# Optimization experiments

Hardware: AMD Instinct MI355X
Metric: run time of the kernel (lower is better)

Reference implementation:

```python
import jax, jax.numpy as jnp
import numpy as np

LAMBDA_CONT = 0.01
SIGMA = 1.0


def _pairwise_dist(x):
    # Euclidean cdist(x, x): [N, N]
    sq = jnp.sum(x * x, axis=-1)  # [N]
    d2 = sq[:, None] + sq[None, :] - 2.0 * (x @ x.T)
    d2 = jnp.maximum(d2, 0.0)
    # safe sqrt (grad 0 at 0, matching torch.cdist subgradient)
    return jnp.where(d2 > 0, jnp.sqrt(jnp.where(d2 > 0, d2, 1.0)), 0.0)


def setup_inputs() -> dict:
    key = jax.random.key(0)
    k1, k2 = jax.random.split(key)
    points = jax.random.normal(k1, (8192, 2), dtype=jnp.float32)
    outputs = jax.random.uniform(k2, (8192, 8), dtype=jnp.float32)
    return {"points": points, "outputs": outputs}


def reference(points, outputs):
    n = points.shape[0]
    dist = _pairwise_dist(points)                     # [N, N]
    weights = jnp.exp(-(dist * dist) / (2.0 * SIGMA ** 2))
    weights = weights * (1.0 - jnp.eye(n, dtype=points.dtype))
    diff = _pairwise_dist(outputs)                    # [N, N]
    loss = jnp.sum(weights * diff) / (n * (n - 1))
    return LAMBDA_CONT * loss
```

## Files before the change

kernel.cpp:

```cpp
#include <hip/hip_runtime.h>


typedef float v2f __attribute__((ext_vector_type(2)));
typedef float v4f __attribute__((ext_vector_type(4)));
typedef _Float16 h4 __attribute__((ext_vector_type(4)));
typedef float f32x4 __attribute__((ext_vector_type(4)));

constexpr int N_PTS  = 8192;
constexpr int T16    = N_PTS / 16;
constexpr int TDIM   = N_PTS / 64;
constexpr int NTILES = TDIM * (TDIM + 1) / 2;
constexpr int WPB    = 4;
constexpr int NBLOCKS = NTILES / WPB;

constexpr float KE = -0.72134752044448169f;
constexpr float M2 =  1.4426950408889634f;

__device__ __forceinline__ int tri_before(int r) {
    return r * TDIM - (r * (r - 1)) / 2;
}

__global__ __launch_bounds__(256) void cont_prep(
    const float* __restrict__ points, const float* __restrict__ outputs,
    h4* __restrict__ AO, h4* __restrict__ AP,
    h4* __restrict__ BO, h4* __restrict__ BP)
{
    const int idx = blockIdx.x * 256 + threadIdx.x;
    const int l  = idx & 63;
    const int t  = idx >> 6;
    const int q  = l >> 4, cl = l & 15;
    const int row = t * 16 + cl;

    const v4f* o = reinterpret_cast<const v4f*>(outputs + 8 * row);
    const v4f x = o[0], y = o[1];
    const v4f s = x * x + y * y;
    const float on = (s.x + s.y) + (s.z + s.w);
    const v2f p = reinterpret_cast<const v2f*>(points)[row];
    const float pn = p.x * p.x + p.y * p.y;

    const _Float16 h0 = (_Float16)0.f, h1 = (_Float16)1.f;
    h4 ao, ap, bo, bp;
    if (q == 0)      ao = h4{(_Float16)x.x, (_Float16)x.y, (_Float16)x.z, (_Float16)x.w};
    else if (q == 1) ao = h4{(_Float16)y.x, (_Float16)y.y, (_Float16)y.z, (_Float16)y.w};
    else if (q == 2) ao = h4{(_Float16)on, h1, h0, h0};
    else             ao = h4{h0, h0, h0, h0};
    if (q == 0) ap = h4{(_Float16)p.x, (_Float16)p.y, (_Float16)(KE * pn), h1};
    else        ap = h4{h0, h0, h0, h0};
    if (q == 0)      bo = h4{(_Float16)(-2.f * x.x), (_Float16)(-2.f * x.y),
                             (_Float16)(-2.f * x.z), (_Float16)(-2.f * x.w)};
    else if (q == 1) bo = h4{(_Float16)(-2.f * y.x), (_Float16)(-2.f * y.y),
                             (_Float16)(-2.f * y.z), (_Float16)(-2.f * y.w)};
    else if (q == 2) bo = h4{h1, (_Float16)on, h0, h0};
    else             bo = h4{h0, h0, h0, h0};
    if (q == 0) bp = h4{(_Float16)(M2 * p.x), (_Float16)(M2 * p.y), h1,
                        (_Float16)(KE * pn)};
    else        bp = h4{h0, h0, h0, h0};

    AO[idx] = ao; AP[idx] = ap; BO[idx] = bo; BP[idx] = bp;
}

__global__ __launch_bounds__(256, 4) void cont_pairs(
    const h4* __restrict__ AO, const h4* __restrict__ AP,
    const h4* __restrict__ BO, const h4* __restrict__ BP,
    double* __restrict__ partials)
{
    const int tid  = threadIdx.x;
    const int wid  = tid >> 6;
    const int lane = tid & 63;
    const int g    = blockIdx.x * WPB + wid;

    int ti = (int)((2 * TDIM + 1 -
                    sqrtf((float)((2 * TDIM + 1) * (2 * TDIM + 1) - 8 * g))) * 0.5f);
    ti = ti < 0 ? 0 : (ti > TDIM - 1 ? TDIM - 1 : ti);
    while (tri_before(ti + 1) <= g) ++ti;
    while (tri_before(ti) > g) --ti;
    const int tj = ti + (g - tri_before(ti));
    const bool diag = (ti == tj);

    const int q = lane >> 4, cl = lane & 15;

    h4 aO[4], aP[4], bO[4], bP[4];
    #pragma unroll
    for (int it = 0; it < 4; ++it) {
        const int ta = (ti * 4 + it) * 64 + lane;
        aO[it] = AO[ta]; aP[it] = AP[ta];
        const int tb = (tj * 4 + it) * 64 + lane;
        bO[it] = BO[tb]; bP[it] = BP[tb];
    }

    float accE[4] = {0.f, 0.f, 0.f, 0.f};

    #pragma unroll
    for (int jt = 0; jt < 4; ++jt) {
        const int jcol = jt * 16 + cl;
        #pragma unroll
        for (int it = 0; it < 4; ++it) {
            const f32x4 z = {0.f, 0.f, 0.f, 0.f};
            f32x4 dO = __builtin_amdgcn_mfma_f32_16x16x16f16(aO[it], bO[jt], z, 0, 0, 0);
            f32x4 dP = __builtin_amdgcn_mfma_f32_16x16x16f16(aP[it], bP[jt], z, 0, 0, 0);
            #pragma unroll
            for (int e = 0; e < 4; ++e) {
                float diff = __builtin_amdgcn_sqrtf(fmaxf(dO[e], 0.f));
                if (diag) {
                    const int irow = it * 16 + q * 4 + e;
                    diff = (jcol > irow) ? diff : 0.f;
                }
                accE[e] = fmaf(__builtin_amdgcn_exp2f(dP[e]), diff, accE[e]);
            }
        }
    }

    float accS = (accE[0] + accE[1]) + (accE[2] + accE[3]);
    #pragma unroll
    for (int off = 32; off > 0; off >>= 1)
        accS += __shfl_down(accS, off, 64);

    __shared__ float wpart[WPB];
    if (lane == 0) wpart[wid] = accS;
    __syncthreads();
    if (tid == 0) {
        double d = 0.0;
        #pragma unroll
        for (int w = 0; w < WPB; ++w) d += (double)wpart[w];
        partials[blockIdx.x] = d;
    }
}

__global__ __launch_bounds__(1024) void cont_final(
    const double* __restrict__ partials, int nparts,
    float* __restrict__ out, double scale)
{
    const int tid = threadIdx.x;
    double sum = 0.0;
    for (int i = tid; i < nparts; i += 1024) sum += partials[i];
    #pragma unroll
    for (int off = 32; off > 0; off >>= 1)
        sum += __shfl_down(sum, off, 64);

    __shared__ double ws[1024 / 64];
    if ((tid & 63) == 0) ws[tid >> 6] = sum;
    __syncthreads();
    if (tid == 0) {
        double t = 0.0;
        #pragma unroll
        for (int w = 0; w < 1024 / 64; ++w) t += ws[w];
        out[0] = (float)(t * scale);
    }
}

extern "C" void kernel_launch(void* const* d_in, const int* in_sizes, int n_in,
                              void* d_out, int out_size, void* d_ws, size_t ws_size,
                              hipStream_t stream) {
    const float* points  = (const float*)d_in[0];
    const float* outputs = (const float*)d_in[1];
    float* out = (float*)d_out;

    const int n = in_sizes[0] / 2;
    constexpr size_t TBL = (size_t)T16 * 64 * sizeof(h4);
    h4* AO = (h4*)d_ws;
    h4* AP = (h4*)((char*)d_ws + TBL);
    h4* BO = (h4*)((char*)d_ws + 2 * TBL);
    h4* BP = (h4*)((char*)d_ws + 3 * TBL);
    double* partials = (double*)((char*)d_ws + 4 * TBL);

    cont_prep<<<dim3(T16 * 64 / 256), dim3(256), 0, stream>>>(
        points, outputs, AO, AP, BO, BP);
    cont_pairs<<<dim3(NBLOCKS), dim3(256), 0, stream>>>(AO, AP, BO, BP, partials);

    const double scale = 0.01 * 2.0 / ((double)n * (double)(n - 1));
    cont_final<<<1, 1024, 0, stream>>>(partials, NBLOCKS, out, scale);
}
```

Before: 23.19 us.

## Use 64x128 wave tiles over upper triangle and fold final reduction into atomics

Each wave now covers a 64-row by 128-column tile of the upper triangle, with a new index mapping that pairs row tiles, instead of a 64x64 tile. This halves the number of waves and amortizes the A-fragment loads and per-wave setup over twice the MFMA work. The separate final reduction kernel is removed: each block scales its partial and atomically adds it to the float output, which is zeroed by a memset. This trades a kernel launch for float atomics, which can change summation order and precision.

Result: slower. 31.82 us (+37.2%).

```diff
diff --git a/kernel.cpp b/kernel.cpp
--- a/kernel.cpp
+++ b/kernel.cpp
@@ -8,17 +8,14 @@
 
 constexpr int N_PTS  = 8192;
 constexpr int T16    = N_PTS / 16;
-constexpr int TDIM   = N_PTS / 64;
-constexpr int NTILES = TDIM * (TDIM + 1) / 2;
+constexpr int NWAVES = 4160;
 constexpr int WPB    = 4;
-constexpr int NBLOCKS = NTILES / WPB;
+constexpr int NBLOCKS = NWAVES / WPB;
 
 constexpr float KE = -0.72134752044448169f;
 constexpr float M2 =  1.4426950408889634f;
 
-__device__ __forceinline__ int tri_before(int r) {
-    return r * TDIM - (r * (r - 1)) / 2;
-}
+__device__ __forceinline__ int rp_before(int h) { return h * (129 - h); }
 
 __global__ __launch_bounds__(256) void cont_prep(
     const float* __restrict__ points, const float* __restrict__ outputs,
@@ -62,37 +59,43 @@
 __global__ __launch_bounds__(256, 4) void cont_pairs(
     const h4* __restrict__ AO, const h4* __restrict__ AP,
     const h4* __restrict__ BO, const h4* __restrict__ BP,
-    double* __restrict__ partials)
+    float* __restrict__ out, double scale)
 {
     const int tid  = threadIdx.x;
     const int wid  = tid >> 6;
     const int lane = tid & 63;
     const int g    = blockIdx.x * WPB + wid;
 
-    int ti = (int)((2 * TDIM + 1 -
-                    sqrtf((float)((2 * TDIM + 1) * (2 * TDIM + 1) - 8 * g))) * 0.5f);
-    ti = ti < 0 ? 0 : (ti > TDIM - 1 ? TDIM - 1 : ti);
-    while (tri_before(ti + 1) <= g) ++ti;
-    while (tri_before(ti) > g) --ti;
-    const int tj = ti + (g - tri_before(ti));
-    const bool diag = (ti == tj);
+    int h = (int)((129.f - sqrtf(16641.f - 4.f * (float)g)) * 0.5f);
+    h = h < 0 ? 0 : (h > 63 ? 63 : h);
+    while (rp_before(h + 1) <= g) ++h;
+    while (rp_before(h) > g) --h;
+    const int r2  = g - rp_before(h);
+    const int spr = 64 - h;
+    const int ri  = 2 * h + r2 / spr;
+    const int cs  = h + r2 % spr;
+    const bool straddle = (cs == (ri >> 1));
 
     const int q = lane >> 4, cl = lane & 15;
+    const int rowbase = ri * 64, colbase = cs * 128;
 
-    h4 aO[4], aP[4], bO[4], bP[4];
+    h4 aO[4], aP[4], bO[8], bP[8];
     #pragma unroll
     for (int it = 0; it < 4; ++it) {
-        const int ta = (ti * 4 + it) * 64 + lane;
+        const int ta = (ri * 4 + it) * 64 + lane;
         aO[it] = AO[ta]; aP[it] = AP[ta];
-        const int tb = (tj * 4 + it) * 64 + lane;
-        bO[it] = BO[tb]; bP[it] = BP[tb];
+    }
+    #pragma unroll
+    for (int jt = 0; jt < 8; ++jt) {
+        const int tb = (cs * 8 + jt) * 64 + lane;
+        bO[jt] = BO[tb]; bP[jt] = BP[tb];
     }
 
     float accE[4] = {0.f, 0.f, 0.f, 0.f};
 
     #pragma unroll
-    for (int jt = 0; jt < 4; ++jt) {
-        const int jcol = jt * 16 + cl;
+    for (int jt = 0; jt < 8; ++jt) {
+        const int jcol = colbase + jt * 16 + cl;
         #pragma unroll
         for (int it = 0; it < 4; ++it) {
             const f32x4 z = {0.f, 0.f, 0.f, 0.f};
@@ -101,8 +104,8 @@
             #pragma unroll
             for (int e = 0; e < 4; ++e) {
                 float diff = __builtin_amdgcn_sqrtf(fmaxf(dO[e], 0.f));
-                if (diag) {
-                    const int irow = it * 16 + q * 4 + e;
+                if (straddle) {
+                    const int irow = rowbase + it * 16 + q * 4 + e;
                     diff = (jcol > irow) ? diff : 0.f;
                 }
                 accE[e] = fmaf(__builtin_amdgcn_exp2f(dP[e]), diff, accE[e]);
@@ -122,29 +125,7 @@
         double d = 0.0;
         #pragma unroll
         for (int w = 0; w < WPB; ++w) d += (double)wpart[w];
-        partials[blockIdx.x] = d;
-    }
-}
-
-__global__ __launch_bounds__(1024) void cont_final(
-    const double* __restrict__ partials, int nparts,
-    float* __restrict__ out, double scale)
-{
-    const int tid = threadIdx.x;
-    double sum = 0.0;
-    for (int i = tid; i < nparts; i += 1024) sum += partials[i];
-    #pragma unroll
-    for (int off = 32; off > 0; off >>= 1)
-        sum += __shfl_down(sum, off, 64);
-
-    __shared__ double ws[1024 / 64];
-    if ((tid & 63) == 0) ws[tid >> 6] = sum;
-    __syncthreads();
-    if (tid == 0) {
-        double t = 0.0;
-        #pragma unroll
-        for (int w = 0; w < 1024 / 64; ++w) t += ws[w];
-        out[0] = (float)(t * scale);
+        atomicAdd(out, (float)(d * scale));
     }
 }
 
@@ -161,12 +142,13 @@
     h4* AP = (h4*)((char*)d_ws + TBL);
     h4* BO = (h4*)((char*)d_ws + 2 * TBL);
     h4* BP = (h4*)((char*)d_ws + 3 * TBL);
-    double* partials = (double*)((char*)d_ws + 4 * TBL);
+
+    hipMemsetAsync(d_out, 0, sizeof(float), stream);
 
     cont_prep<<<dim3(T16 * 64 / 256), dim3(256), 0, stream>>>(
         points, outputs, AO, AP, BO, BP);
-    cont_pairs<<<dim3(NBLOCKS), dim3(256), 0, stream>>>(AO, AP, BO, BP, partials);
 
     const double scale = 0.01 * 2.0 / ((double)n * (double)(n - 1));
-    cont_final<<<1, 1024, 0, stream>>>(partials, NBLOCKS, out, scale);
+    cont_pairs<<<dim3(NBLOCKS), dim3(256), 0, stream>>>(
+        AO, AP, BO, BP, out, scale);
 }
```
